# Optimization experiments

Measured on AMD Instinct MI355X. Metric: run time of the kernel, lower is better.

Reference implementation:

```python
import jax, jax.numpy as jnp
import numpy as np

N = 20000
E = 640000
IN_CH = 256
HID = 128
OUT_CH = 64
HEADS = 8
C1 = HID // HEADS   # 16 per-head dim, layer 1 (concat)
C2 = OUT_CH         # 64 per-head dim, layer 2 (head mean)
NEG_SLOPE = 0.2


def gat_conv(x, edge_index, W, a_src, a_dst, b, concat):
    """PyG GATConv (no self loops, eval mode / no dropout).
    W: [F_in, H*C], a_src/a_dst: [H, C], b: [H*C] or [C]."""
    H, C = a_src.shape
    h = (x @ W).reshape(-1, H, C)                      # [N, H, C]
    s_src = jnp.einsum('nhc,hc->nh', h, a_src)         # [N, H]
    s_dst = jnp.einsum('nhc,hc->nh', h, a_dst)         # [N, H]
    src, dst = edge_index[0], edge_index[1]
    e = jax.nn.leaky_relu(s_src[src] + s_dst[dst], NEG_SLOPE)  # [E, H]
    # segment softmax over incoming edges of each destination node
    m = jax.ops.segment_max(e, dst, num_segments=N)    # [N, H] (-inf for isolated)
    p = jnp.exp(e - m[dst])                            # [E, H]
    z = jax.ops.segment_sum(p, dst, num_segments=N)    # [N, H]
    alpha = p / z[dst]                                 # [E, H]
    out = jax.ops.segment_sum(h[src] * alpha[..., None], dst, num_segments=N)  # [N,H,C]
    out = out.reshape(-1, H * C) if concat else out.mean(axis=1)
    return out + b


def hetero_layer(x, edge_indices, Ws, a_srcs, a_dsts, bs, concat):
    # HeteroConv(aggr='mean') over edge types targeting 'user'
    outs = [gat_conv(x, edge_indices[t], Ws[t], a_srcs[t], a_dsts[t], bs[t], concat)
            for t in range(len(edge_indices))]
    return sum(outs) / len(outs)


def setup_inputs() -> dict:
    key = jax.random.key(0)
    ks = jax.random.split(key, 16)
    g = 0.1
    return {
        'x': jax.random.normal(ks[0], (N, IN_CH), dtype=jnp.float32),
        'edge_index_a': jax.random.randint(ks[1], (2, E), 0, N, dtype=jnp.int32).astype(jnp.int64),
        'edge_index_b': jax.random.randint(ks[2], (2, E), 0, N, dtype=jnp.int32).astype(jnp.int64),
        # layer 1 params, stacked over 2 edge types
        'W1': jax.random.normal(ks[3], (2, IN_CH, HEADS * C1), dtype=jnp.float32) * g,
        'a1_src': jax.random.normal(ks[4], (2, HEADS, C1), dtype=jnp.float32) * g,
        'a1_dst': jax.random.normal(ks[5], (2, HEADS, C1), dtype=jnp.float32) * g,
        'b1': jnp.zeros((2, HEADS * C1), dtype=jnp.float32),
        # layer 2 params
        'W2': jax.random.normal(ks[6], (2, HID, HEADS * C2), dtype=jnp.float32) * g,
        'a2_src': jax.random.normal(ks[7], (2, HEADS, C2), dtype=jnp.float32) * g,
        'a2_dst': jax.random.normal(ks[8], (2, HEADS, C2), dtype=jnp.float32) * g,
        'b2': jnp.zeros((2, C2), dtype=jnp.float32),
        # classifier
        'Wc1': jax.random.normal(ks[9], (OUT_CH, 32), dtype=jnp.float32) * g,
        'bc1': jnp.zeros((32,), dtype=jnp.float32),
        'Wc2': jax.random.normal(ks[10], (32, 2), dtype=jnp.float32) * g,
        'bc2': jnp.zeros((2,), dtype=jnp.float32),
    }


def reference(x, edge_index_a, edge_index_b, W1, a1_src, a1_dst, b1,
              W2, a2_src, a2_dst, b2, Wc1, bc1, Wc2, bc2):
    eis = [edge_index_a, edge_index_b]
    h = hetero_layer(x, eis, W1, a1_src, a1_dst, b1, concat=True)   # [N, 128]
    h = jax.nn.elu(h)  # (dropout is identity in eval mode)
    h = hetero_layer(h, eis, W2, a2_src, a2_dst, b2, concat=False)  # [N, 64]
    h = jax.nn.elu(h)
    logits = jax.nn.relu(h @ Wc1 + bc1) @ Wc2 + bc2                 # [N, 2]
    return logits
```

## Files before the change

kernel.cpp:

```cpp
#include <hip/hip_runtime.h>
#include <math.h>

#define NN 20000
#define EE 640000
#define NB 157
#define BCAP 5120
#define NBLK 160
#define CHNK 4000

__device__ __forceinline__ void wave_fence() {
  __builtin_amdgcn_wave_barrier();
  asm volatile("s_waitcnt lgkmcnt(0)" ::: "memory");
  __builtin_amdgcn_wave_barrier();
}

__global__ __launch_bounds__(256) void bin_k(const int* __restrict__ ea,
                                             const int* __restrict__ eb,
                                             int* __restrict__ gcnt,
                                             int* __restrict__ bbuf) {
  int t = blockIdx.y;
  const int* ei = t ? eb : ea;
  int tid = threadIdx.x;
  __shared__ int lh[NB], lbase[NB];
  if (tid < NB) lh[tid] = 0;
  __syncthreads();
  int e0 = blockIdx.x * CHNK;
  int e1 = min(e0 + CHNK, EE);
  int myb[16], myr[16], myv[16];
#pragma unroll
  for (int i = 0; i < 16; ++i) {
    int e = e0 + tid + i * 256;
    if (e < e1) {
      int s = ei[e], d = ei[EE + e];
      int b = d >> 7;
      myb[i] = b;
      myv[i] = (s << 7) | (d & 127);
      myr[i] = atomicAdd(&lh[b], 1);
    } else {
      myb[i] = -1;
    }
  }
  __syncthreads();
  if (tid < NB) {
    int c = lh[tid];
    lbase[tid] = c ? atomicAdd(&gcnt[t * NB + tid], c) : 0;
  }
  __syncthreads();
#pragma unroll
  for (int i = 0; i < 16; ++i) {
    int b = myb[i];
    if (b >= 0) {
      int pos = lbase[b] + myr[i];
      if (pos < BCAP) bbuf[((size_t)t * NB + b) * BCAP + pos] = myv[i];
    }
  }
}

__global__ __launch_bounds__(512) void bscan_k(const int* __restrict__ gcnt,
                                               int* __restrict__ bstart) {
  __shared__ int buf[512];
  int tid = threadIdx.x;
  int t = tid >> 8, b = tid & 255;
  int val = (b < NB) ? gcnt[t * NB + b] : 0;
  buf[tid] = val;
  __syncthreads();
  for (int s = 1; s < 256; s <<= 1) {
    int x = ((tid & 255) >= s) ? buf[tid - s] : 0;
    __syncthreads();
    buf[tid] += x;
    __syncthreads();
  }
  if (b < NB) bstart[t * NB + b] = buf[tid] - val;
}

__global__ __launch_bounds__(256) void build_k(const int* __restrict__ gcnt,
                                               const int* __restrict__ bstart,
                                               const int* __restrict__ bbuf,
                                               int* __restrict__ rowptr,
                                               int* __restrict__ csr) {
  int b = blockIdx.x, t = blockIdx.y;
  int cnt = gcnt[t * NB + b];
  int start = bstart[t * NB + b];
  int n0 = b << 7;
  int nlocal = min(128, NN - n0);
  int tid = threadIdx.x;
  __shared__ int arr[128], lcur[128];
  if (tid < 128) arr[tid] = 0;
  __syncthreads();
  const int* ebuf = bbuf + ((size_t)t * NB + b) * BCAP;
  for (int i = tid; i < cnt; i += 256) atomicAdd(&arr[ebuf[i] & 127], 1);
  __syncthreads();
  int deg = (tid < 128) ? arr[tid] : 0;
  for (int s = 1; s < 128; s <<= 1) {
    int x = (tid < 128 && tid >= s) ? arr[tid - s] : 0;
    __syncthreads();
    if (tid < 128) arr[tid] += x;
    __syncthreads();
  }
  if (tid < nlocal) {
    int incl = arr[tid];
    rowptr[t * (NN + 1) + n0 + tid + 1] = start + incl;
    lcur[tid] = start + incl - deg;
  }
  if (b == 0 && tid == 0) rowptr[t * (NN + 1)] = 0;
  __syncthreads();
  for (int i = tid; i < cnt; i += 256) {
    int v = ebuf[i];
    int pos = atomicAdd(&lcur[v & 127], 1);
    csr[(size_t)t * EE + pos] = v >> 7;
  }
}

template <int NT, int BM, int BN, int BK, int TM, int TN>
__global__ __launch_bounds__(NT) void sgemm_k(const float* __restrict__ A,
                                              const float* __restrict__ B,
                                              float* __restrict__ C, int M, int N, int K,
                                              long long Abs, long long Bbs, long long Cbs) {
  A += blockIdx.z * Abs; B += blockIdx.z * Bbs; C += blockIdx.z * Cbs;
  const int bm = blockIdx.x * BM, bn = blockIdx.y * BN;
  __shared__ float As[BK][BM + 4];
  __shared__ float Bs[BK][BN + 4];
  int tid = threadIdx.x;
  constexpr int TX = BN / TN;
  int tx = tid % TX, ty = tid / TX;
  float acc[TM][TN] = {};
  for (int k0 = 0; k0 < K; k0 += BK) {
#pragma unroll
    for (int i = 0; i < (BM * BK) / (NT * 4); ++i) {
      int idx = tid + i * NT;
      int row = idx / (BK / 4), kq = idx % (BK / 4);
      float4 v = make_float4(0.f, 0.f, 0.f, 0.f);
      int gr = bm + row;
      if (gr < M) v = *(const float4*)&A[(size_t)gr * K + k0 + kq * 4];
      As[kq * 4 + 0][row] = v.x; As[kq * 4 + 1][row] = v.y;
      As[kq * 4 + 2][row] = v.z; As[kq * 4 + 3][row] = v.w;
    }
#pragma unroll
    for (int i = 0; i < (BK * BN) / (NT * 4); ++i) {
      int idx = tid + i * NT;
      int row = idx / (BN / 4), cq = idx % (BN / 4);
      *(float4*)&Bs[row][cq * 4] = *(const float4*)&B[(size_t)(k0 + row) * N + bn + cq * 4];
    }
    __syncthreads();
#pragma unroll
    for (int k = 0; k < BK; ++k) {
      float a[TM], b[TN];
#pragma unroll
      for (int i = 0; i < TM; i += 4) *(float4*)&a[i] = *(float4*)&As[k][ty * TM + i];
#pragma unroll
      for (int j = 0; j < TN; j += 4) *(float4*)&b[j] = *(float4*)&Bs[k][tx * TN + j];
#pragma unroll
      for (int i = 0; i < TM; ++i)
#pragma unroll
        for (int j = 0; j < TN; ++j) acc[i][j] += a[i] * b[j];
    }
    __syncthreads();
  }
#pragma unroll
  for (int i = 0; i < TM; ++i) {
    int gr = bm + ty * TM + i;
    if (gr < M) {
#pragma unroll
      for (int j = 0; j < TN; j += 4)
        *(float4*)&C[(size_t)gr * N + bn + tx * TN + j] = *(float4*)&acc[i][j];
    }
  }
}

template <int NT, int BM, int BK, int TM, int TN, int KC>
__global__ __launch_bounds__(NT) void sgemm_splitk_k(const float* __restrict__ A,
                                                     const float* __restrict__ B,
                                                     float* __restrict__ P, int M, int K) {
  const int N = 64;
  const int bm = blockIdx.x * BM;
  const int k0base = blockIdx.y * KC;
  P += (size_t)blockIdx.y * M * N;
  __shared__ float As[BK][BM + 4];
  __shared__ float Bs[BK][N + 4];
  int tid = threadIdx.x;
  constexpr int TX = N / TN;
  int tx = tid % TX, ty = tid / TX;
  float acc[TM][TN] = {};
  for (int k0 = k0base; k0 < k0base + KC; k0 += BK) {
#pragma unroll
    for (int i = 0; i < (BM * BK) / (NT * 4); ++i) {
      int idx = tid + i * NT;
      int row = idx / (BK / 4), kq = idx % (BK / 4);
      float4 v = make_float4(0.f, 0.f, 0.f, 0.f);
      int gr = bm + row;
      if (gr < M) v = *(const float4*)&A[(size_t)gr * K + k0 + kq * 4];
      As[kq * 4 + 0][row] = v.x; As[kq * 4 + 1][row] = v.y;
      As[kq * 4 + 2][row] = v.z; As[kq * 4 + 3][row] = v.w;
    }
#pragma unroll
    for (int i = 0; i < (BK * N) / (NT * 4); ++i) {
      int idx = tid + i * NT;
      int row = idx / (N / 4), cq = idx % (N / 4);
      *(float4*)&Bs[row][cq * 4] = *(const float4*)&B[(size_t)(k0 + row) * N + cq * 4];
    }
    __syncthreads();
#pragma unroll
    for (int k = 0; k < BK; ++k) {
      float a[TM], b[TN];
#pragma unroll
      for (int i = 0; i < TM; i += 4) *(float4*)&a[i] = *(float4*)&As[k][ty * TM + i];
#pragma unroll
      for (int j = 0; j < TN; j += 4) *(float4*)&b[j] = *(float4*)&Bs[k][tx * TN + j];
#pragma unroll
      for (int i = 0; i < TM; ++i)
#pragma unroll
        for (int j = 0; j < TN; ++j) acc[i][j] += a[i] * b[j];
    }
    __syncthreads();
  }
#pragma unroll
  for (int i = 0; i < TM; ++i) {
    int gr = bm + ty * TM + i;
    if (gr < M) {
#pragma unroll
      for (int j = 0; j < TN; j += 4)
        *(float4*)&P[(size_t)gr * N + tx * TN + j] = *(float4*)&acc[i][j];
    }
  }
}

template <int C>
__global__ void score_k(const float* __restrict__ hf, const float* __restrict__ as_,
                        const float* __restrict__ ad_, float* __restrict__ ss,
                        float* __restrict__ sd) {
  int idx = blockIdx.x * 256 + threadIdx.x;
  if (idx >= 2 * NN * 8) return;
  int t = idx / (NN * 8), r = idx % (NN * 8), n = r / 8, hh = r % 8;
  const int HC = 8 * C;
  const float* hrow = hf + (size_t)t * NN * HC + (size_t)n * HC + hh * C;
  const float* a1 = as_ + t * HC + hh * C;
  const float* a2 = ad_ + t * HC + hh * C;
  float s1 = 0.f, s2 = 0.f;
#pragma unroll
  for (int c = 0; c < C; c += 4) {
    float4 f = *(const float4*)&hrow[c];
    float4 u = *(const float4*)&a1[c];
    float4 w = *(const float4*)&a2[c];
    s1 += f.x * u.x + f.y * u.y + f.z * u.z + f.w * u.w;
    s2 += f.x * w.x + f.y * w.y + f.z * w.z + f.w * w.w;
  }
  ss[idx] = s1; sd[idx] = s2;
}

__device__ __forceinline__ float lrelu(float v) { return v > 0.f ? v : 0.2f * v; }

__global__ __launch_bounds__(256) void aggw1_k(const int* __restrict__ rowptr,
                                               const int* __restrict__ csr,
                                               const float* __restrict__ ssrc,
                                               const float* __restrict__ sdst,
                                               const float* __restrict__ h,
                                               float* __restrict__ out) {
  int t = blockIdx.y;
  rowptr += t * (NN + 1); csr += (size_t)t * EE;
  ssrc += (size_t)t * NN * 8; sdst += (size_t)t * NN * 8;
  h += (size_t)t * NN * 128; out += (size_t)t * NN * 128;
  int tid = threadIdx.x, w = tid >> 6, lane = tid & 63;
  int n = blockIdx.x * 4 + w;
  int row = rowptr[n], end = rowptr[n + 1];
  __shared__ int sidx[4][64];
  __shared__ float sexp[4][64][8];
  float4 sda = *(const float4*)&sdst[(size_t)n * 8];
  float4 sdb = *(const float4*)&sdst[(size_t)n * 8 + 4];
  float za_x = 0.f, za_y = 0.f, za_z = 0.f, za_w = 0.f;
  float zb_x = 0.f, zb_y = 0.f, zb_z = 0.f, zb_w = 0.f;
  int hme = lane >> 3;
  float2 acc = make_float2(0.f, 0.f);
  for (int base = row; base < end; base += 64) {
    int cnt = min(64, end - base);
    if (lane < cnt) {
      int s = csr[base + lane];
      sidx[w][lane] = s;
      float4 pa = *(const float4*)&ssrc[(size_t)s * 8];
      float4 pb = *(const float4*)&ssrc[(size_t)s * 8 + 4];
      float4 ea, eb;
      ea.x = __expf(lrelu(pa.x + sda.x)); ea.y = __expf(lrelu(pa.y + sda.y));
      ea.z = __expf(lrelu(pa.z + sda.z)); ea.w = __expf(lrelu(pa.w + sda.w));
      eb.x = __expf(lrelu(pb.x + sdb.x)); eb.y = __expf(lrelu(pb.y + sdb.y));
      eb.z = __expf(lrelu(pb.z + sdb.z)); eb.w = __expf(lrelu(pb.w + sdb.w));
      za_x += ea.x; za_y += ea.y; za_z += ea.z; za_w += ea.w;
      zb_x += eb.x; zb_y += eb.y; zb_z += eb.z; zb_w += eb.w;
      *(float4*)&sexp[w][lane][0] = ea;
      *(float4*)&sexp[w][lane][4] = eb;
    }
    wave_fence();
    for (int e = 0; e < cnt; ++e) {
      int s = sidx[w][e];
      float a = sexp[w][e][hme];
      float2 v = *(const float2*)&h[(size_t)s * 128 + lane * 2];
      acc.x += a * v.x; acc.y += a * v.y;
    }
    wave_fence();
  }
#pragma unroll
  for (int off = 32; off; off >>= 1) {
    za_x += __shfl_xor(za_x, off); za_y += __shfl_xor(za_y, off);
    za_z += __shfl_xor(za_z, off); za_w += __shfl_xor(za_w, off);
    zb_x += __shfl_xor(zb_x, off); zb_y += __shfl_xor(zb_y, off);
    zb_z += __shfl_xor(zb_z, off); zb_w += __shfl_xor(zb_w, off);
  }
  float zh[8] = {za_x, za_y, za_z, za_w, zb_x, zb_y, zb_z, zb_w};
  float z = zh[hme];
  float iz = z > 0.f ? 1.f / z : 0.f;
  acc.x *= iz; acc.y *= iz;
  *(float2*)&out[(size_t)n * 128 + lane * 2] = acc;
}

__global__ void combine1_k(const float* __restrict__ oa, const float* __restrict__ ob,
                           const float* __restrict__ b1, float* __restrict__ hmid) {
  int idx = blockIdx.x * 256 + threadIdx.x;
  if (idx >= NN * 128) return;
  int j = idx & 127;
  float v = 0.5f * ((oa[idx] + b1[j]) + (ob[idx] + b1[128 + j]));
  hmid[idx] = v > 0.f ? v : (__expf(v) - 1.f);
}

__global__ void fold2_k(const float* __restrict__ W2, const float* __restrict__ a2s,
                        const float* __restrict__ a2d, float* __restrict__ wsf,
                        float* __restrict__ wdf) {
  int idx = blockIdx.x * 256 + threadIdx.x;
  if (idx >= 2048) return;
  int t = idx >> 10, r = idx & 1023, hh = r >> 7, k = r & 127;
  const float* wrow = W2 + (size_t)t * 65536 + (size_t)k * 512 + hh * 64;
  const float* as = a2s + t * 512 + hh * 64;
  const float* ad = a2d + t * 512 + hh * 64;
  float s1 = 0.f, s2 = 0.f;
  for (int c = 0; c < 64; ++c) { s1 += wrow[c] * as[c]; s2 += wrow[c] * ad[c]; }
  wsf[idx] = s1; wdf[idx] = s2;
}

__global__ void foldB_k(const float* __restrict__ W2, float* __restrict__ Bmat) {
  int idx = blockIdx.x * 256 + threadIdx.x;
  if (idx >= 131072) return;
  int t = idx >> 16, r = idx & 65535, rowr = r >> 6, c = r & 63;
  int hh = rowr >> 7, k = rowr & 127;
  Bmat[idx] = 0.125f * W2[(size_t)t * 65536 + (size_t)k * 512 + hh * 64 + c];
}

__global__ void score2_k(const float* __restrict__ hmid, const float* __restrict__ wsf,
                         const float* __restrict__ wdf, float* __restrict__ ss,
                         float* __restrict__ sdo) {
  int idx = blockIdx.x * 256 + threadIdx.x;
  if (idx >= NN * 8) return;
  int n = idx >> 3, hh = idx & 7;
  const float* hm = hmid + (size_t)n * 128;
  const float* w0s = wsf + (size_t)hh * 128;
  const float* w0d = wdf + (size_t)hh * 128;
  const float* w1s = wsf + (size_t)(8 + hh) * 128;
  const float* w1d = wdf + (size_t)(8 + hh) * 128;
  float s0s = 0.f, s0d = 0.f, s1s = 0.f, s1d = 0.f;
#pragma unroll
  for (int c = 0; c < 128; c += 4) {
    float4 f = *(const float4*)&hm[c];
    float4 a = *(const float4*)&w0s[c];
    float4 b = *(const float4*)&w0d[c];
    float4 u = *(const float4*)&w1s[c];
    float4 v = *(const float4*)&w1d[c];
    s0s += f.x * a.x + f.y * a.y + f.z * a.z + f.w * a.w;
    s0d += f.x * b.x + f.y * b.y + f.z * b.z + f.w * b.w;
    s1s += f.x * u.x + f.y * u.y + f.z * u.z + f.w * u.w;
    s1d += f.x * v.x + f.y * v.y + f.z * v.z + f.w * v.w;
  }
  ss[idx] = s0s; sdo[idx] = s0d;
  ss[NN * 8 + idx] = s1s; sdo[NN * 8 + idx] = s1d;
}

__global__ __launch_bounds__(256) void aggw2_k(const int* __restrict__ rowptr,
                                               const int* __restrict__ csr,
                                               const float* __restrict__ ssrc,
                                               const float* __restrict__ sdst,
                                               const float* __restrict__ hmid,
                                               float* __restrict__ agg, int t) {
  rowptr += t * (NN + 1); csr += (size_t)t * EE;
  ssrc += (size_t)t * NN * 8; sdst += (size_t)t * NN * 8;
  int tid = threadIdx.x, w = tid >> 6, lane = tid & 63;
  int n = blockIdx.x * 4 + w;
  int row = rowptr[n], end = rowptr[n + 1];
  __shared__ int sidx[4][64];
  __shared__ float sexp[4][64][8];
  float4 sda = *(const float4*)&sdst[(size_t)n * 8];
  float4 sdb = *(const float4*)&sdst[(size_t)n * 8 + 4];
  float za_x = 0.f, za_y = 0.f, za_z = 0.f, za_w = 0.f;
  float zb_x = 0.f, zb_y = 0.f, zb_z = 0.f, zb_w = 0.f;
  float2 acc[8];
#pragma unroll
  for (int i = 0; i < 8; ++i) acc[i] = make_float2(0.f, 0.f);
  for (int base = row; base < end; base += 64) {
    int cnt = min(64, end - base);
    if (lane < cnt) {
      int s = csr[base + lane];
      sidx[w][lane] = s;
      float4 pa = *(const float4*)&ssrc[(size_t)s * 8];
      float4 pb = *(const float4*)&ssrc[(size_t)s * 8 + 4];
      float4 ea, eb;
      ea.x = __expf(lrelu(pa.x + sda.x)); ea.y = __expf(lrelu(pa.y + sda.y));
      ea.z = __expf(lrelu(pa.z + sda.z)); ea.w = __expf(lrelu(pa.w + sda.w));
      eb.x = __expf(lrelu(pb.x + sdb.x)); eb.y = __expf(lrelu(pb.y + sdb.y));
      eb.z = __expf(lrelu(pb.z + sdb.z)); eb.w = __expf(lrelu(pb.w + sdb.w));
      za_x += ea.x; za_y += ea.y; za_z += ea.z; za_w += ea.w;
      zb_x += eb.x; zb_y += eb.y; zb_z += eb.z; zb_w += eb.w;
      *(float4*)&sexp[w][lane][0] = ea;
      *(float4*)&sexp[w][lane][4] = eb;
    }
    wave_fence();
    for (int e = 0; e < cnt; ++e) {
      int s = sidx[w][e];
      float4 ea = *(const float4*)&sexp[w][e][0];
      float4 eb = *(const float4*)&sexp[w][e][4];
      float2 v = *(const float2*)&hmid[(size_t)s * 128 + lane * 2];
      acc[0].x += ea.x * v.x; acc[0].y += ea.x * v.y;
      acc[1].x += ea.y * v.x; acc[1].y += ea.y * v.y;
      acc[2].x += ea.z * v.x; acc[2].y += ea.z * v.y;
      acc[3].x += ea.w * v.x; acc[3].y += ea.w * v.y;
      acc[4].x += eb.x * v.x; acc[4].y += eb.x * v.y;
      acc[5].x += eb.y * v.x; acc[5].y += eb.y * v.y;
      acc[6].x += eb.z * v.x; acc[6].y += eb.z * v.y;
      acc[7].x += eb.w * v.x; acc[7].y += eb.w * v.y;
    }
    wave_fence();
  }
#pragma unroll
  for (int off = 32; off; off >>= 1) {
    za_x += __shfl_xor(za_x, off); za_y += __shfl_xor(za_y, off);
    za_z += __shfl_xor(za_z, off); za_w += __shfl_xor(za_w, off);
    zb_x += __shfl_xor(zb_x, off); zb_y += __shfl_xor(zb_y, off);
    zb_z += __shfl_xor(zb_z, off); zb_w += __shfl_xor(zb_w, off);
  }
  float zh[8] = {za_x, za_y, za_z, za_w, zb_x, zb_y, zb_z, zb_w};
#pragma unroll
  for (int i = 0; i < 8; ++i) {
    float z = zh[i];
    float iz = z > 0.f ? 1.f / z : 0.f;
    float2 o = make_float2(acc[i].x * iz, acc[i].y * iz);
    *(float2*)&agg[(size_t)n * 1024 + i * 128 + lane * 2] = o;
  }
}

__global__ void combine2p_k(const float* __restrict__ P, const float* __restrict__ b2,
                            float* __restrict__ feat) {
  int idx = blockIdx.x * 256 + threadIdx.x;
  if (idx >= NN * 16) return;
  int n = idx >> 4, j = (idx & 15) * 4;
  const size_t SZ = (size_t)NN * 64;
  size_t o = (size_t)n * 64 + j;
  float4 sa = make_float4(0.f, 0.f, 0.f, 0.f), sb = sa;
#pragma unroll
  for (int k = 0; k < 4; ++k) {
    float4 va = *(const float4*)&P[k * SZ + o];
    float4 vb = *(const float4*)&P[(4 + k) * SZ + o];
    sa.x += va.x; sa.y += va.y; sa.z += va.z; sa.w += va.w;
    sb.x += vb.x; sb.y += vb.y; sb.z += vb.z; sb.w += vb.w;
  }
  float4 ba = *(const float4*)&b2[j];
  float4 bb = *(const float4*)&b2[64 + j];
  float4 v;
  v.x = 0.5f * ((sa.x + ba.x) + (sb.x + bb.x));
  v.y = 0.5f * ((sa.y + ba.y) + (sb.y + bb.y));
  v.z = 0.5f * ((sa.z + ba.z) + (sb.z + bb.z));
  v.w = 0.5f * ((sa.w + ba.w) + (sb.w + bb.w));
  v.x = v.x > 0.f ? v.x : (__expf(v.x) - 1.f);
  v.y = v.y > 0.f ? v.y : (__expf(v.y) - 1.f);
  v.z = v.z > 0.f ? v.z : (__expf(v.z) - 1.f);
  v.w = v.w > 0.f ? v.w : (__expf(v.w) - 1.f);
  *(float4*)&feat[o] = v;
}

__global__ __launch_bounds__(256) void cls_k(const float* __restrict__ feat,
                                             const float* __restrict__ Wc1,
                                             const float* __restrict__ bc1,
                                             const float* __restrict__ Wc2,
                                             const float* __restrict__ bc2,
                                             float* __restrict__ out) {
  __shared__ float w1[64 * 32];
  __shared__ float w2[64];
  __shared__ float b1s[32], b2s[2];
  __shared__ float fs[8 * 64];
  __shared__ float hs[8 * 32];
  int tid = threadIdx.x;
  for (int i = tid; i < 2048; i += 256) w1[i] = Wc1[i];
  if (tid < 64) w2[tid] = Wc2[tid];
  if (tid < 32) b1s[tid] = bc1[tid];
  if (tid < 2) b2s[tid] = bc2[tid];
  int nbase = blockIdx.x * 8;
  for (int i = tid; i < 512; i += 256) fs[i] = feat[(size_t)nbase * 64 + i];
  __syncthreads();
  int local = tid >> 5, tt = tid & 31;
  const float* f = fs + local * 64;
  float acc = b1s[tt];
#pragma unroll
  for (int c = 0; c < 64; ++c) acc += f[c] * w1[c * 32 + tt];
  hs[local * 32 + tt] = fmaxf(acc, 0.f);
  __syncthreads();
  if (tid < 16) {
    int l = tid >> 1, j = tid & 1;
    float o = b2s[j];
#pragma unroll
    for (int i = 0; i < 32; ++i) o += hs[l * 32 + i] * w2[i * 2 + j];
    out[(size_t)(nbase + l) * 2 + j] = o;
  }
}

extern "C" void kernel_launch(void* const* d_in, const int* in_sizes, int n_in,
                              void* d_out, int out_size, void* d_ws, size_t ws_size,
                              hipStream_t stream) {
  const float* x   = (const float*)d_in[0];
  const int* eia   = (const int*)d_in[1];
  const int* eib   = (const int*)d_in[2];
  const float* W1  = (const float*)d_in[3];
  const float* a1s = (const float*)d_in[4];
  const float* a1d = (const float*)d_in[5];
  const float* b1  = (const float*)d_in[6];
  const float* W2  = (const float*)d_in[7];
  const float* a2s = (const float*)d_in[8];
  const float* a2d = (const float*)d_in[9];
  const float* b2  = (const float*)d_in[10];
  const float* Wc1 = (const float*)d_in[11];
  const float* bc1 = (const float*)d_in[12];
  const float* Wc2 = (const float*)d_in[13];
  const float* bc2 = (const float*)d_in[14];
  float* out = (float*)d_out;

  char* ws = (char*)d_ws;
  size_t off = 0;
  auto alloc = [&](size_t bytes) -> char* {
    char* p = ws + off;
    off += (bytes + 255) & ~(size_t)255;
    return p;
  };
  int* gcnt    = (int*)alloc((size_t)2 * NB * 4);
  int* bstart  = (int*)alloc((size_t)2 * NB * 4);
  int* bbuf    = (int*)alloc((size_t)2 * NB * BCAP * 4);
  int* rowptr  = (int*)alloc((size_t)2 * (NN + 1) * 4);
  int* csr     = (int*)alloc((size_t)2 * EE * 4);
  float* h1    = (float*)alloc((size_t)2 * NN * 128 * 4);
  float* s1s   = (float*)alloc((size_t)2 * NN * 8 * 4);
  float* s1d   = (float*)alloc((size_t)2 * NN * 8 * 4);
  float* o1    = (float*)alloc((size_t)2 * NN * 128 * 4);
  float* hmid  = (float*)alloc((size_t)NN * 128 * 4);
  float* wsf   = (float*)alloc((size_t)2048 * 4);
  float* wdf   = (float*)alloc((size_t)2048 * 4);
  float* Bmat  = (float*)alloc((size_t)131072 * 4);
  float* s2s   = (float*)alloc((size_t)2 * NN * 8 * 4);
  float* s2d   = (float*)alloc((size_t)2 * NN * 8 * 4);
  float* aggb  = (float*)alloc((size_t)NN * 1024 * 4);
  float* pbuf  = (float*)alloc((size_t)8 * NN * 64 * 4);
  float* feat  = (float*)alloc((size_t)NN * 64 * 4);

  hipMemsetAsync(gcnt, 0, (size_t)2 * NB * 4, stream);
  bin_k<<<dim3(NBLK, 2), 256, 0, stream>>>(eia, eib, gcnt, bbuf);
  bscan_k<<<1, 512, 0, stream>>>(gcnt, bstart);
  build_k<<<dim3(NB, 2), 256, 0, stream>>>(gcnt, bstart, bbuf, rowptr, csr);

  fold2_k<<<8, 256, 0, stream>>>(W2, a2s, a2d, wsf, wdf);
  foldB_k<<<512, 256, 0, stream>>>(W2, Bmat);

  sgemm_k<256, 64, 128, 32, 8, 4><<<dim3((NN + 63) / 64, 1, 2), 256, 0, stream>>>(
      x, W1, h1, NN, 128, 256, 0LL, 256LL * 128, (long long)NN * 128);
  score_k<16><<<(2 * NN * 8 + 255) / 256, 256, 0, stream>>>(h1, a1s, a1d, s1s, s1d);
  aggw1_k<<<dim3(NN / 4, 2), 256, 0, stream>>>(rowptr, csr, s1s, s1d, h1, o1);
  combine1_k<<<(NN * 128 + 255) / 256, 256, 0, stream>>>(o1, o1 + (size_t)NN * 128, b1, hmid);

  score2_k<<<(NN * 8 + 255) / 256, 256, 0, stream>>>(hmid, wsf, wdf, s2s, s2d);
  for (int t = 0; t < 2; ++t) {
    aggw2_k<<<NN / 4, 256, 0, stream>>>(rowptr, csr, s2s, s2d, hmid, aggb, t);
    sgemm_splitk_k<256, 64, 32, 4, 4, 256><<<dim3((NN + 63) / 64, 4), 256, 0, stream>>>(
        aggb, Bmat + (size_t)t * 65536, pbuf + (size_t)t * 4 * NN * 64, NN, 1024);
  }
  combine2p_k<<<(NN * 16 + 255) / 256, 256, 0, stream>>>(pbuf, b2, feat);

  cls_k<<<NN / 8, 256, 0, stream>>>(feat, Wc1, bc1, Wc2, bc2, out);
}
```

Baseline: 521.9 us.

## Gather node features in bf16 for both GAT aggregation kernels

Adds bf16 copies of the layer-1 projected features and the layer-1 output, made by a new cast kernel and by combine1_k. Both aggregation kernels now gather these packed bf16 pairs instead of fp32 float2, which halves the bytes of the random per-edge row gathers. Separately, the first sgemm drops its N tile from 128 to 64 and doubles the grid in y. The cost is an extra cast pass, extra writes, and reduced precision in the aggregated features.

```diff
diff --git a/kernel.cpp b/kernel.cpp
--- a/kernel.cpp
+++ b/kernel.cpp
@@ -1,4 +1,5 @@
 #include <hip/hip_runtime.h>
+#include <hip/hip_bf16.h>
 #include <math.h>
 
 #define NN 20000
@@ -12,6 +13,18 @@
   __builtin_amdgcn_wave_barrier();
   asm volatile("s_waitcnt lgkmcnt(0)" ::: "memory");
   __builtin_amdgcn_wave_barrier();
+}
+
+__device__ __forceinline__ unsigned pack_bf2(float a, float b) {
+  __hip_bfloat162 h2 = __float22bfloat162_rn(make_float2(a, b));
+  return *(unsigned*)&h2;
+}
+__device__ __forceinline__ float2 unpack_bf2(unsigned v) {
+  float2 r;
+  unsigned lo = v << 16, hi = v & 0xffff0000u;
+  r.x = __uint_as_float(lo);
+  r.y = __uint_as_float(hi);
+  return r;
 }
 
 __global__ __launch_bounds__(256) void bin_k(const int* __restrict__ ea,
@@ -247,18 +260,25 @@
   ss[idx] = s1; sd[idx] = s2;
 }
 
+__global__ void cast_k(const float* __restrict__ h, unsigned* __restrict__ hb, int n2) {
+  int idx = blockIdx.x * 256 + threadIdx.x;
+  if (idx >= n2) return;
+  float2 v = *(const float2*)&h[(size_t)idx * 2];
+  hb[idx] = pack_bf2(v.x, v.y);
+}
+
 __device__ __forceinline__ float lrelu(float v) { return v > 0.f ? v : 0.2f * v; }
 
 __global__ __launch_bounds__(256) void aggw1_k(const int* __restrict__ rowptr,
                                                const int* __restrict__ csr,
                                                const float* __restrict__ ssrc,
                                                const float* __restrict__ sdst,
-                                               const float* __restrict__ h,
+                                               const unsigned* __restrict__ hb,
                                                float* __restrict__ out) {
   int t = blockIdx.y;
   rowptr += t * (NN + 1); csr += (size_t)t * EE;
   ssrc += (size_t)t * NN * 8; sdst += (size_t)t * NN * 8;
-  h += (size_t)t * NN * 128; out += (size_t)t * NN * 128;
+  hb += (size_t)t * NN * 64; out += (size_t)t * NN * 128;
   int tid = threadIdx.x, w = tid >> 6, lane = tid & 63;
   int n = blockIdx.x * 4 + w;
   int row = rowptr[n], end = rowptr[n + 1];
@@ -291,7 +311,7 @@
     for (int e = 0; e < cnt; ++e) {
       int s = sidx[w][e];
       float a = sexp[w][e][hme];
-      float2 v = *(const float2*)&h[(size_t)s * 128 + lane * 2];
+      float2 v = unpack_bf2(hb[(size_t)s * 64 + lane]);
       acc.x += a * v.x; acc.y += a * v.y;
     }
     wave_fence();
@@ -311,12 +331,19 @@
 }
 
 __global__ void combine1_k(const float* __restrict__ oa, const float* __restrict__ ob,
-                           const float* __restrict__ b1, float* __restrict__ hmid) {
+                           const float* __restrict__ b1, float* __restrict__ hmid,
+                           unsigned* __restrict__ hmidb) {
   int idx = blockIdx.x * 256 + threadIdx.x;
-  if (idx >= NN * 128) return;
-  int j = idx & 127;
-  float v = 0.5f * ((oa[idx] + b1[j]) + (ob[idx] + b1[128 + j]));
-  hmid[idx] = v > 0.f ? v : (__expf(v) - 1.f);
+  if (idx >= NN * 64) return;
+  int n = idx >> 6, j2 = idx & 63, j = j2 * 2;
+  float2 va = *(const float2*)&oa[(size_t)n * 128 + j];
+  float2 vb = *(const float2*)&ob[(size_t)n * 128 + j];
+  float vx = 0.5f * ((va.x + b1[j]) + (vb.x + b1[128 + j]));
+  float vy = 0.5f * ((va.y + b1[j + 1]) + (vb.y + b1[128 + j + 1]));
+  vx = vx > 0.f ? vx : (__expf(vx) - 1.f);
+  vy = vy > 0.f ? vy : (__expf(vy) - 1.f);
+  *(float2*)&hmid[(size_t)n * 128 + j] = make_float2(vx, vy);
+  hmidb[idx] = pack_bf2(vx, vy);
 }
 
 __global__ void fold2_k(const float* __restrict__ W2, const float* __restrict__ a2s,
@@ -373,7 +400,7 @@
                                                const int* __restrict__ csr,
                                                const float* __restrict__ ssrc,
                                                const float* __restrict__ sdst,
-                                               const float* __restrict__ hmid,
+                                               const unsigned* __restrict__ hmidb,
                                                float* __restrict__ agg, int t) {
   rowptr += t * (NN + 1); csr += (size_t)t * EE;
   ssrc += (size_t)t * NN * 8; sdst += (size_t)t * NN * 8;
@@ -411,7 +438,7 @@
       int s = sidx[w][e];
       float4 ea = *(const float4*)&sexp[w][e][0];
       float4 eb = *(const float4*)&sexp[w][e][4];
-      float2 v = *(const float2*)&hmid[(size_t)s * 128 + lane * 2];
+      float2 v = unpack_bf2(hmidb[(size_t)s * 64 + lane]);
       acc[0].x += ea.x * v.x; acc[0].y += ea.x * v.y;
       acc[1].x += ea.y * v.x; acc[1].y += ea.y * v.y;
       acc[2].x += ea.z * v.x; acc[2].y += ea.z * v.y;
@@ -531,24 +558,26 @@
     off += (bytes + 255) & ~(size_t)255;
     return p;
   };
-  int* gcnt    = (int*)alloc((size_t)2 * NB * 4);
-  int* bstart  = (int*)alloc((size_t)2 * NB * 4);
-  int* bbuf    = (int*)alloc((size_t)2 * NB * BCAP * 4);
-  int* rowptr  = (int*)alloc((size_t)2 * (NN + 1) * 4);
-  int* csr     = (int*)alloc((size_t)2 * EE * 4);
-  float* h1    = (float*)alloc((size_t)2 * NN * 128 * 4);
-  float* s1s   = (float*)alloc((size_t)2 * NN * 8 * 4);
-  float* s1d   = (float*)alloc((size_t)2 * NN * 8 * 4);
-  float* o1    = (float*)alloc((size_t)2 * NN * 128 * 4);
-  float* hmid  = (float*)alloc((size_t)NN * 128 * 4);
-  float* wsf   = (float*)alloc((size_t)2048 * 4);
-  float* wdf   = (float*)alloc((size_t)2048 * 4);
-  float* Bmat  = (float*)alloc((size_t)131072 * 4);
-  float* s2s   = (float*)alloc((size_t)2 * NN * 8 * 4);
-  float* s2d   = (float*)alloc((size_t)2 * NN * 8 * 4);
-  float* aggb  = (float*)alloc((size_t)NN * 1024 * 4);
-  float* pbuf  = (float*)alloc((size_t)8 * NN * 64 * 4);
-  float* feat  = (float*)alloc((size_t)NN * 64 * 4);
+  int* gcnt       = (int*)alloc((size_t)2 * NB * 4);
+  int* bstart     = (int*)alloc((size_t)2 * NB * 4);
+  int* bbuf       = (int*)alloc((size_t)2 * NB * BCAP * 4);
+  int* rowptr     = (int*)alloc((size_t)2 * (NN + 1) * 4);
+  int* csr        = (int*)alloc((size_t)2 * EE * 4);
+  float* h1       = (float*)alloc((size_t)2 * NN * 128 * 4);
+  unsigned* h1b   = (unsigned*)alloc((size_t)2 * NN * 64 * 4);
+  float* s1s      = (float*)alloc((size_t)2 * NN * 8 * 4);
+  float* s1d      = (float*)alloc((size_t)2 * NN * 8 * 4);
+  float* o1       = (float*)alloc((size_t)2 * NN * 128 * 4);
+  float* hmid     = (float*)alloc((size_t)NN * 128 * 4);
+  unsigned* hmidb = (unsigned*)alloc((size_t)NN * 64 * 4);
+  float* wsf      = (float*)alloc((size_t)2048 * 4);
+  float* wdf      = (float*)alloc((size_t)2048 * 4);
+  float* Bmat     = (float*)alloc((size_t)131072 * 4);
+  float* s2s      = (float*)alloc((size_t)2 * NN * 8 * 4);
+  float* s2d      = (float*)alloc((size_t)2 * NN * 8 * 4);
+  float* aggb     = (float*)alloc((size_t)NN * 1024 * 4);
+  float* pbuf     = (float*)alloc((size_t)8 * NN * 64 * 4);
+  float* feat     = (float*)alloc((size_t)NN * 64 * 4);
 
   hipMemsetAsync(gcnt, 0, (size_t)2 * NB * 4, stream);
   bin_k<<<dim3(NBLK, 2), 256, 0, stream>>>(eia, eib, gcnt, bbuf);
@@ -558,15 +587,16 @@
   fold2_k<<<8, 256, 0, stream>>>(W2, a2s, a2d, wsf, wdf);
   foldB_k<<<512, 256, 0, stream>>>(W2, Bmat);
 
-  sgemm_k<256, 64, 128, 32, 8, 4><<<dim3((NN + 63) / 64, 1, 2), 256, 0, stream>>>(
+  sgemm_k<256, 64, 64, 32, 4, 4><<<dim3((NN + 63) / 64, 2, 2), 256, 0, stream>>>(
       x, W1, h1, NN, 128, 256, 0LL, 256LL * 128, (long long)NN * 128);
   score_k<16><<<(2 * NN * 8 + 255) / 256, 256, 0, stream>>>(h1, a1s, a1d, s1s, s1d);
-  aggw1_k<<<dim3(NN / 4, 2), 256, 0, stream>>>(rowptr, csr, s1s, s1d, h1, o1);
-  combine1_k<<<(NN * 128 + 255) / 256, 256, 0, stream>>>(o1, o1 + (size_t)NN * 128, b1, hmid);
+  cast_k<<<(2 * NN * 64 + 255) / 256, 256, 0, stream>>>(h1, h1b, 2 * NN * 64);
+  aggw1_k<<<dim3(NN / 4, 2), 256, 0, stream>>>(rowptr, csr, s1s, s1d, h1b, o1);
+  combine1_k<<<(NN * 64 + 255) / 256, 256, 0, stream>>>(o1, o1 + (size_t)NN * 128, b1, hmid, hmidb);
 
   score2_k<<<(NN * 8 + 255) / 256, 256, 0, stream>>>(hmid, wsf, wdf, s2s, s2d);
   for (int t = 0; t < 2; ++t) {
-    aggw2_k<<<NN / 4, 256, 0, stream>>>(rowptr, csr, s2s, s2d, hmid, aggb, t);
+    aggw2_k<<<NN / 4, 256, 0, stream>>>(rowptr, csr, s2s, s2d, hmidb, aggb, t);
     sgemm_splitk_k<256, 64, 32, 4, 4, 256><<<dim3((NN + 63) / 64, 4), 256, 0, stream>>>(
         aggb, Bmat + (size_t)t * 65536, pbuf + (size_t)t * 4 * NN * 64, NN, 1024);
   }
```

Result: faster. 465.6 us (-10.8%).
